# Kernel optimization log

Hardware: AMD Instinct MI355X
Metric: run time of the kernel (lower is better)

Reference implementation:

```python
import jax, jax.numpy as jnp
import numpy as np

CH, H, N, N_SSM, SEQ_L = 1, 1024, 64, 1024, 2048


def setup_inputs() -> dict:
    key = jax.random.key(0)
    ks = jax.random.split(key, 5)
    return {
        "C_ri": jax.random.normal(ks[0], (CH, H, N, 2), dtype=jnp.float32),
        "log_dt": jax.random.normal(ks[1], (H,), dtype=jnp.float32),
        "B_ri": jax.random.normal(ks[2], (N_SSM, N, 2), dtype=jnp.float32),
        "inv_A_real": jax.random.normal(ks[3], (N_SSM, N), dtype=jnp.float32),
        "A_imag": jax.random.normal(ks[4], (N_SSM, N), dtype=jnp.float32),
        "L": SEQ_L,
    }


def _kernel(C_ri, log_dt, B_ri, inv_A_real, A_imag, L):
    # Reconstruct complex params from real views (torch view_as_complex)
    C = C_ri[..., 0] + 1j * C_ri[..., 1]        # (CH, H, N) complex64
    B = B_ri[..., 0] + 1j * B_ri[..., 1]        # (n_ssm, N)
    A = -jnp.exp(inv_A_real) + 1j * A_imag      # (n_ssm, N), Re(A) < 0

    rep = log_dt.shape[0] // inv_A_real.shape[0]  # H // n_ssm
    B = jnp.tile(B, (rep, 1))                   # 't n -> (v t) n' : (H, N)
    A = jnp.tile(A, (rep, 1))                   # (H, N)

    dt = jnp.exp(log_dt)                        # (H,), rate = 1.0
    dtA = A * dt[:, None]                       # (H, N)

    # C <- B * C * dt / (1 - dtA/2)   (bilinear discretization of input/output)
    Ct = (B[None] * C) / (1.0 - dtA / 2) * dt[:, None]   # (CH, H, N)
    dA = (1.0 + dtA / 2) / (1.0 - dtA / 2)      # (H, N), |dA| < 1
    dA_log = jnp.log(dA)                        # (H, N)

    # log-Vandermonde: K[c,h,l] = 2 * Re( sum_n Ct[c,h,n] * exp(dA_log[h,n] * l) )
    l = jnp.arange(L, dtype=jnp.float32)
    V = jnp.exp(dA_log[:, :, None] * l)         # (H, N, L) complex
    K = 2.0 * jnp.einsum('chn,hnl->chl', Ct, V).real  # (CH, H, L)
    return K


def reference(C_ri, log_dt, B_ri, inv_A_real, A_imag, L):
    # state=None path: returns (K, K_state=None); we return K
    return _kernel(C_ri, log_dt, B_ri, inv_A_real, A_imag, L)
```

## Files before the change

### kernel.cpp

```cpp
#include <hip/hip_runtime.h>
#include <math.h>

#define CH 1
#define H 1024
#define NN 64
#define N_SSM 1024
#define SEQ_L 2048
#define TPB 256
#define LPT 8

typedef float v2f __attribute__((ext_vector_type(2)));

__global__ __launch_bounds__(TPB) void sskd_kernel(
    const float* __restrict__ C_ri, const float* __restrict__ log_dt,
    const float* __restrict__ B_ri, const float* __restrict__ inv_A_real,
    const float* __restrict__ A_imag, float* __restrict__ out)
{
    const int h   = blockIdx.x;
    const int tid = threadIdx.x;

    __shared__ __align__(8) float sCtr[NN], sCti[NN], sCdr[NN], sCdi[NN],
                                  sP[NN], sQ[NN], sLogr[NN], sThrev[NN];

    if (tid < NN) {
        const int n = tid;
        const float dt  = __expf(log_dt[h]);
        const float Ar  = -__expf(inv_A_real[h * NN + n]);
        const float Ai  = A_imag[h * NN + n];
        const float dtAr = Ar * dt, dtAi = Ai * dt;
        const float den_r = 1.0f - 0.5f * dtAr;
        const float den_i = -0.5f * dtAi;
        const float num_r = 1.0f + 0.5f * dtAr;
        const float num_i = 0.5f * dtAi;
        const float inv_den = 1.0f / (den_r * den_r + den_i * den_i);
        const float dA_r = (num_r * den_r + num_i * den_i) * inv_den;
        const float dA_i = (num_i * den_r - num_r * den_i) * inv_den;
        const int   bh = h % N_SSM;
        const float Br = B_ri[(bh * NN + n) * 2 + 0];
        const float Bi = B_ri[(bh * NN + n) * 2 + 1];
        const float Cr = C_ri[(h * NN + n) * 2 + 0];
        const float Ci = C_ri[(h * NN + n) * 2 + 1];
        const float BCr = Br * Cr - Bi * Ci;
        const float BCi = Br * Ci + Bi * Cr;
        const float sc = 2.0f * dt * inv_den;
        const float ctr = (BCr * den_r + BCi * den_i) * sc;
        const float cti = (BCi * den_r - BCr * den_i) * sc;
        sCtr[n] = ctr;
        sCti[n] = cti;
        sCdr[n] = ctr * dA_r - cti * dA_i;
        sCdi[n] = ctr * dA_i + cti * dA_r;
        const float q = dA_r * dA_r + dA_i * dA_i;
        sP[n] = 2.0f * dA_r;
        sQ[n] = q;
        sLogr[n]  = fmaxf(0.5f * __logf(q), -1.0e30f);
        sThrev[n] = atan2f(dA_i, dA_r) * 0.15915494309189535f;
    }
    __syncthreads();

    const float l0 = (float)(tid * LPT);
    v2f acc[LPT];
    #pragma unroll
    for (int k = 0; k < LPT; ++k) acc[k] = (v2f)(0.0f);

    #pragma unroll 2
    for (int m = 0; m < NN / 2; ++m) {
        const v2f logr  = *(const v2f*)&sLogr[2 * m];
        const v2f threv = *(const v2f*)&sThrev[2 * m];
        v2f e;
        e.x = __expf(logr.x * l0);
        e.y = __expf(logr.y * l0);
        v2f ph = threv * l0;
        ph.x -= floorf(ph.x);
        ph.y -= floorf(ph.y);
        float snx, csx, sny, csy;
        __sincosf(ph.x * 6.283185307179586f, &snx, &csx);
        __sincosf(ph.y * 6.283185307179586f, &sny, &csy);
        v2f wr, wi;
        wr.x = e.x * csx; wr.y = e.y * csy;
        wi.x = e.x * snx; wi.y = e.y * sny;

        const v2f ctr = *(const v2f*)&sCtr[2 * m];
        const v2f cti = *(const v2f*)&sCti[2 * m];
        const v2f cdr = *(const v2f*)&sCdr[2 * m];
        const v2f cdi = *(const v2f*)&sCdi[2 * m];
        const v2f p   = *(const v2f*)&sP[2 * m];
        const v2f q   = *(const v2f*)&sQ[2 * m];

        v2f x2 = ctr * wr - cti * wi;
        v2f x1 = cdr * wr - cdi * wi;
        acc[0] += x2;
        acc[1] += x1;
        #pragma unroll
        for (int k = 2; k < LPT; ++k) {
            const v2f xn = p * x1 - q * x2;
            acc[k] += xn;
            x2 = x1;
            x1 = xn;
        }
    }

    float4 o0, o1;
    o0.x = acc[0].x + acc[0].y;
    o0.y = acc[1].x + acc[1].y;
    o0.z = acc[2].x + acc[2].y;
    o0.w = acc[3].x + acc[3].y;
    o1.x = acc[4].x + acc[4].y;
    o1.y = acc[5].x + acc[5].y;
    o1.z = acc[6].x + acc[6].y;
    o1.w = acc[7].x + acc[7].y;
    float4* o = (float4*)(out + (size_t)h * SEQ_L + tid * LPT);
    o[0] = o0;
    o[1] = o1;
}

extern "C" void kernel_launch(void* const* d_in, const int* in_sizes, int n_in,
                              void* d_out, int out_size, void* d_ws, size_t ws_size,
                              hipStream_t stream) {
    const float* C_ri       = (const float*)d_in[0];
    const float* log_dt     = (const float*)d_in[1];
    const float* B_ri       = (const float*)d_in[2];
    const float* inv_A_real = (const float*)d_in[3];
    const float* A_imag     = (const float*)d_in[4];
    float* out = (float*)d_out;

    sskd_kernel<<<dim3(H), dim3(TPB), 0, stream>>>(
        C_ri, log_dt, B_ri, inv_A_real, A_imag, out);
}
```

Measured before the change: 78.20 us.

## Replace per-thread exp/sincos with precomputed power tables via repeated squaring

Each thread's starting power dA^(8*tid) is now built as the product of a coarse power (dA^(128*t1)) and a fine power (dA^(8*t0)), both precomputed into shared-memory tables by repeated complex squaring. This drops the per-term expf, floorf and sincos transcendentals from the inner loop and replaces them with extra shared-memory loads. The cost is a second table-building phase, an extra barrier and more LDS traffic. Forming high powers by repeated squaring can also lose accuracy compared with the log/exp form.

```diff
diff --git a/kernel.cpp b/kernel.cpp
--- a/kernel.cpp
+++ b/kernel.cpp
@@ -8,6 +8,7 @@
 #define SEQ_L 2048
 #define TPB 256
 #define LPT 8
+#define TSTR 68
 
 typedef float v2f __attribute__((ext_vector_type(2)));
 
@@ -19,8 +20,12 @@
     const int h   = blockIdx.x;
     const int tid = threadIdx.x;
 
-    __shared__ __align__(8) float sCtr[NN], sCti[NN], sCdr[NN], sCdi[NN],
-                                  sP[NN], sQ[NN], sLogr[NN], sThrev[NN];
+    __shared__ __align__(16) float sU1r[16][TSTR], sU1i[16][TSTR];
+    __shared__ __align__(16) float sVdr[16][TSTR], sVdi[16][TSTR];
+    __shared__ __align__(16) float sT0r[16][TSTR], sT0i[16][TSTR];
+    __shared__ __align__(16) float sP[NN], sQ[NN];
+    __shared__ __align__(16) float sW8r[NN], sW8i[NN], sW128r[NN], sW128i[NN];
+    __shared__ __align__(16) float sCtr[NN], sCti[NN], sCdr[NN], sCdi[NN];
 
     if (tid < NN) {
         const int n = tid;
@@ -45,49 +50,85 @@
         const float sc = 2.0f * dt * inv_den;
         const float ctr = (BCr * den_r + BCi * den_i) * sc;
         const float cti = (BCi * den_r - BCr * den_i) * sc;
-        sCtr[n] = ctr;
-        sCti[n] = cti;
+        sCtr[n] = ctr; sCti[n] = cti;
         sCdr[n] = ctr * dA_r - cti * dA_i;
         sCdi[n] = ctr * dA_i + cti * dA_r;
-        const float q = dA_r * dA_r + dA_i * dA_i;
         sP[n] = 2.0f * dA_r;
-        sQ[n] = q;
-        sLogr[n]  = fmaxf(0.5f * __logf(q), -1.0e30f);
-        sThrev[n] = atan2f(dA_i, dA_r) * 0.15915494309189535f;
+        sQ[n] = dA_r * dA_r + dA_i * dA_i;
+        float wr = dA_r * dA_r - dA_i * dA_i, wi = 2.0f * dA_r * dA_i;
+        float tr = wr * wr - wi * wi,         ti = 2.0f * wr * wi;
+        wr = tr * tr - ti * ti;               wi = 2.0f * tr * ti;
+        sW8r[n] = wr; sW8i[n] = wi;
+        tr = wr * wr - wi * wi;               ti = 2.0f * wr * wi;
+        wr = tr * tr - ti * ti;               wi = 2.0f * tr * ti;
+        tr = wr * wr - wi * wi;               ti = 2.0f * wr * wi;
+        wr = tr * tr - ti * ti;               wi = 2.0f * tr * ti;
+        sW128r[n] = wr; sW128i[n] = wi;
     }
     __syncthreads();
 
-    const float l0 = (float)(tid * LPT);
+    {
+        const int n = tid & 63;
+        const int g = tid >> 6;
+        {
+            const float wr = sW128r[n], wi = sW128i[n];
+            const float ctr = sCtr[n], cti = sCti[n];
+            const float cdr = sCdr[n], cdi = sCdi[n];
+            const float b2r = wr*wr - wi*wi,   b2i = 2.0f*wr*wi;
+            const float b4r = b2r*b2r - b2i*b2i, b4i = 2.0f*b2r*b2i;
+            const float b8r = b4r*b4r - b4i*b4i, b8i = 2.0f*b4r*b4i;
+            float Wr = 1.0f, Wi = 0.0f;
+            if (g & 1) { Wr = b4r; Wi = b4i; }
+            if (g & 2) { const float t = Wr*b8r - Wi*b8i; Wi = Wr*b8i + Wi*b8r; Wr = t; }
+            #pragma unroll
+            for (int i = 0; i < 4; ++i) {
+                const int t1 = 4 * g + i;
+                sU1r[t1][n] = ctr*Wr - cti*Wi;
+                sU1i[t1][n] = ctr*Wi + cti*Wr;
+                sVdr[t1][n] = cdr*Wr - cdi*Wi;
+                sVdi[t1][n] = cdr*Wi + cdi*Wr;
+                const float t = Wr*wr - Wi*wi; Wi = Wr*wi + Wi*wr; Wr = t;
+            }
+        }
+        {
+            const float ur = sW8r[n], ui = sW8i[n];
+            const float a2r = ur*ur - ui*ui,     a2i = 2.0f*ur*ui;
+            const float a4r = a2r*a2r - a2i*a2i, a4i = 2.0f*a2r*a2i;
+            const float a8r = a4r*a4r - a4i*a4i, a8i = 2.0f*a4r*a4i;
+            float Vr = 1.0f, Vi = 0.0f;
+            if (g & 1) { Vr = a4r; Vi = a4i; }
+            if (g & 2) { const float t = Vr*a8r - Vi*a8i; Vi = Vr*a8i + Vi*a8r; Vr = t; }
+            #pragma unroll
+            for (int i = 0; i < 4; ++i) {
+                const int t0 = 4 * g + i;
+                sT0r[t0][n] = Vr;
+                sT0i[t0][n] = Vi;
+                const float t = Vr*ur - Vi*ui; Vi = Vr*ui + Vi*ur; Vr = t;
+            }
+        }
+    }
+    __syncthreads();
+
+    const int t1 = tid >> 4;
+    const int t0 = tid & 15;
+
     v2f acc[LPT];
     #pragma unroll
     for (int k = 0; k < LPT; ++k) acc[k] = (v2f)(0.0f);
 
     #pragma unroll 2
     for (int m = 0; m < NN / 2; ++m) {
-        const v2f logr  = *(const v2f*)&sLogr[2 * m];
-        const v2f threv = *(const v2f*)&sThrev[2 * m];
-        v2f e;
-        e.x = __expf(logr.x * l0);
-        e.y = __expf(logr.y * l0);
-        v2f ph = threv * l0;
-        ph.x -= floorf(ph.x);
-        ph.y -= floorf(ph.y);
-        float snx, csx, sny, csy;
-        __sincosf(ph.x * 6.283185307179586f, &snx, &csx);
-        __sincosf(ph.y * 6.283185307179586f, &sny, &csy);
-        v2f wr, wi;
-        wr.x = e.x * csx; wr.y = e.y * csy;
-        wi.x = e.x * snx; wi.y = e.y * sny;
+        const v2f ur = *(const v2f*)&sU1r[t1][2 * m];
+        const v2f ui = *(const v2f*)&sU1i[t1][2 * m];
+        const v2f vr = *(const v2f*)&sVdr[t1][2 * m];
+        const v2f vi = *(const v2f*)&sVdi[t1][2 * m];
+        const v2f br = *(const v2f*)&sT0r[t0][2 * m];
+        const v2f bi = *(const v2f*)&sT0i[t0][2 * m];
+        const v2f p  = *(const v2f*)&sP[2 * m];
+        const v2f q  = *(const v2f*)&sQ[2 * m];
 
-        const v2f ctr = *(const v2f*)&sCtr[2 * m];
-        const v2f cti = *(const v2f*)&sCti[2 * m];
-        const v2f cdr = *(const v2f*)&sCdr[2 * m];
-        const v2f cdi = *(const v2f*)&sCdi[2 * m];
-        const v2f p   = *(const v2f*)&sP[2 * m];
-        const v2f q   = *(const v2f*)&sQ[2 * m];
-
-        v2f x2 = ctr * wr - cti * wi;
-        v2f x1 = cdr * wr - cdi * wi;
+        v2f x2 = ur * br - ui * bi;
+        v2f x1 = vr * br - vi * bi;
         acc[0] += x2;
         acc[1] += x1;
         #pragma unroll
```

Result: faster. 73.56 us (-5.9%).

## Replace per-thread exp/sincos with double-precision power tables and factored complex products

Applied to the files above, without the earlier changes.

Each thread no longer evaluates exp and sincos of dA^l. The kernel now precomputes powers of dA by repeated squaring in double precision and stores them in shared-memory tables. Each starting power is split into a coarse factor (W^256 times C, and a shifted ×W^8 copy) and a fine factor (W^16), so a complex multiply rebuilds the seed and the second-order recurrence runs two interleaved 8-step chains. Threads drop to 128 per block with 16 outputs each. This removes transcendental work and adds ILP, but costs double-precision setup, a second barrier, more LDS traffic and lower occupancy.

```diff
diff --git a/kernel.cpp b/kernel.cpp
--- a/kernel.cpp
+++ b/kernel.cpp
@@ -6,10 +6,13 @@
 #define NN 64
 #define N_SSM 1024
 #define SEQ_L 2048
-#define TPB 256
-#define LPT 8
+#define TPB 128
+#define LPT 16
 
 typedef float v2f __attribute__((ext_vector_type(2)));
+
+__device__ __forceinline__ v2f lo2(const float4 f) { v2f r; r.x = f.x; r.y = f.y; return r; }
+__device__ __forceinline__ v2f hi2(const float4 f) { v2f r; r.x = f.z; r.y = f.w; return r; }
 
 __global__ __launch_bounds__(TPB) void sskd_kernel(
     const float* __restrict__ C_ri, const float* __restrict__ log_dt,
@@ -19,98 +22,155 @@
     const int h   = blockIdx.x;
     const int tid = threadIdx.x;
 
-    __shared__ __align__(8) float sCtr[NN], sCti[NN], sCdr[NN], sCdi[NN],
-                                  sP[NN], sQ[NN], sLogr[NN], sThrev[NN];
+    __shared__ __align__(16) float4 sU1[8][33], sV1[8][33], sU8[8][33], sV8[8][33];
+    __shared__ __align__(16) float4 sT[16][33];
+    __shared__ __align__(16) float4 sPQ[32];
+    __shared__ double sW8r[NN], sW8i[NN], sW16r[NN], sW16i[NN], sW256r[NN], sW256i[NN];
+    __shared__ double sCtr[NN], sCti[NN], sCdr[NN], sCdi[NN];
 
     if (tid < NN) {
         const int n = tid;
-        const float dt  = __expf(log_dt[h]);
-        const float Ar  = -__expf(inv_A_real[h * NN + n]);
-        const float Ai  = A_imag[h * NN + n];
-        const float dtAr = Ar * dt, dtAi = Ai * dt;
-        const float den_r = 1.0f - 0.5f * dtAr;
-        const float den_i = -0.5f * dtAi;
-        const float num_r = 1.0f + 0.5f * dtAr;
-        const float num_i = 0.5f * dtAi;
-        const float inv_den = 1.0f / (den_r * den_r + den_i * den_i);
-        const float dA_r = (num_r * den_r + num_i * den_i) * inv_den;
-        const float dA_i = (num_i * den_r - num_r * den_i) * inv_den;
-        const int   bh = h % N_SSM;
-        const float Br = B_ri[(bh * NN + n) * 2 + 0];
-        const float Bi = B_ri[(bh * NN + n) * 2 + 1];
-        const float Cr = C_ri[(h * NN + n) * 2 + 0];
-        const float Ci = C_ri[(h * NN + n) * 2 + 1];
-        const float BCr = Br * Cr - Bi * Ci;
-        const float BCi = Br * Ci + Bi * Cr;
-        const float sc = 2.0f * dt * inv_den;
-        const float ctr = (BCr * den_r + BCi * den_i) * sc;
-        const float cti = (BCi * den_r - BCr * den_i) * sc;
-        sCtr[n] = ctr;
-        sCti[n] = cti;
-        sCdr[n] = ctr * dA_r - cti * dA_i;
-        sCdi[n] = ctr * dA_i + cti * dA_r;
-        const float q = dA_r * dA_r + dA_i * dA_i;
-        sP[n] = 2.0f * dA_r;
-        sQ[n] = q;
-        sLogr[n]  = fmaxf(0.5f * __logf(q), -1.0e30f);
-        sThrev[n] = atan2f(dA_i, dA_r) * 0.15915494309189535f;
+        const double dt = exp((double)log_dt[h]);
+        const double Ar = -exp((double)inv_A_real[h * NN + n]);
+        const double Ai = (double)A_imag[h * NN + n];
+        const double hr = 0.5 * Ar * dt, hi = 0.5 * Ai * dt;
+        const double den_r = 1.0 - hr, den_i = -hi;
+        const double num_r = 1.0 + hr, num_i = hi;
+        const double inv_den = 1.0 / (den_r * den_r + den_i * den_i);
+        const double dAr = (num_r * den_r + num_i * den_i) * inv_den;
+        const double dAi = (num_i * den_r - num_r * den_i) * inv_den;
+        const int    bh = h % N_SSM;
+        const double Br = B_ri[(bh * NN + n) * 2 + 0];
+        const double Bi = B_ri[(bh * NN + n) * 2 + 1];
+        const double Cr = C_ri[(h * NN + n) * 2 + 0];
+        const double Ci = C_ri[(h * NN + n) * 2 + 1];
+        const double BCr = Br * Cr - Bi * Ci;
+        const double BCi = Br * Ci + Bi * Cr;
+        const double sc = 2.0 * dt * inv_den;
+        const double ctr = (BCr * den_r + BCi * den_i) * sc;
+        const double cti = (BCi * den_r - BCr * den_i) * sc;
+        sCtr[n] = ctr; sCti[n] = cti;
+        sCdr[n] = ctr * dAr - cti * dAi;
+        sCdi[n] = ctr * dAi + cti * dAr;
+        float* pqp = (float*)&sPQ[n >> 1];
+        pqp[(n & 1)]     = (float)(2.0 * dAr);
+        pqp[2 + (n & 1)] = (float)(dAr * dAr + dAi * dAi);
+        double wr = dAr, wi = dAi, tr;
+        tr = wr * wr - wi * wi; wi = 2.0 * wr * wi; wr = tr;
+        tr = wr * wr - wi * wi; wi = 2.0 * wr * wi; wr = tr;
+        tr = wr * wr - wi * wi; wi = 2.0 * wr * wi; wr = tr;
+        sW8r[n] = wr; sW8i[n] = wi;
+        tr = wr * wr - wi * wi; wi = 2.0 * wr * wi; wr = tr;
+        sW16r[n] = wr; sW16i[n] = wi;
+        tr = wr * wr - wi * wi; wi = 2.0 * wr * wi; wr = tr;
+        tr = wr * wr - wi * wi; wi = 2.0 * wr * wi; wr = tr;
+        tr = wr * wr - wi * wi; wi = 2.0 * wr * wi; wr = tr;
+        tr = wr * wr - wi * wi; wi = 2.0 * wr * wi; wr = tr;
+        sW256r[n] = wr; sW256i[n] = wi;
     }
     __syncthreads();
 
-    const float l0 = (float)(tid * LPT);
+    {
+        const int n = tid & 63;
+        const int g = tid >> 6;
+        const int np = n >> 1, nc = n & 1;
+        {
+            const double ur = sW16r[n], ui = sW16i[n];
+            double Vr = 1.0, Vi = 0.0;
+            if (g) {
+                double ar = ur, ai = ui, t;
+                t = ar * ar - ai * ai; ai = 2.0 * ar * ai; ar = t;
+                t = ar * ar - ai * ai; ai = 2.0 * ar * ai; ar = t;
+                t = ar * ar - ai * ai; ai = 2.0 * ar * ai; ar = t;
+                Vr = ar; Vi = ai;
+            }
+            #pragma unroll
+            for (int i = 0; i < 8; ++i) {
+                float* bp = (float*)&sT[8 * g + i][np];
+                bp[nc] = (float)Vr; bp[2 + nc] = (float)Vi;
+                const double t = Vr * ur - Vi * ui; Vi = Vr * ui + Vi * ur; Vr = t;
+            }
+        }
+        {
+            const double wr = sW256r[n], wi = sW256i[n];
+            const double er = sW8r[n],  ei = sW8i[n];
+            const double ctr = sCtr[n], cti = sCti[n];
+            const double cdr = sCdr[n], cdi = sCdi[n];
+            double Wr = 1.0, Wi = 0.0;
+            if (g) {
+                double ar = wr, ai = wi, t;
+                t = ar * ar - ai * ai; ai = 2.0 * ar * ai; ar = t;
+                t = ar * ar - ai * ai; ai = 2.0 * ar * ai; ar = t;
+                Wr = ar; Wi = ai;
+            }
+            #pragma unroll
+            for (int i = 0; i < 4; ++i) {
+                const int t1 = 4 * g + i;
+                const double u1r = ctr * Wr - cti * Wi, u1i = ctr * Wi + cti * Wr;
+                const double v1r = cdr * Wr - cdi * Wi, v1i = cdr * Wi + cdi * Wr;
+                const double u8r = u1r * er - u1i * ei, u8i = u1r * ei + u1i * er;
+                const double v8r = v1r * er - v1i * ei, v8i = v1r * ei + v1i * er;
+                float* a = (float*)&sU1[t1][np]; a[nc] = (float)u1r; a[2 + nc] = (float)u1i;
+                float* b = (float*)&sV1[t1][np]; b[nc] = (float)v1r; b[2 + nc] = (float)v1i;
+                float* c = (float*)&sU8[t1][np]; c[nc] = (float)u8r; c[2 + nc] = (float)u8i;
+                float* d = (float*)&sV8[t1][np]; d[nc] = (float)v8r; d[2 + nc] = (float)v8i;
+                const double t = Wr * wr - Wi * wi; Wi = Wr * wi + Wi * wr; Wr = t;
+            }
+        }
+    }
+    __syncthreads();
+
+    const int t1 = tid >> 4;
+    const int t0 = tid & 15;
+
     v2f acc[LPT];
     #pragma unroll
     for (int k = 0; k < LPT; ++k) acc[k] = (v2f)(0.0f);
 
+    float4 u1 = sU1[t1][0], v1 = sV1[t1][0], u8 = sU8[t1][0], v8 = sV8[t1][0];
+    float4 tt = sT[t0][0],  pq = sPQ[0];
+
     #pragma unroll 2
     for (int m = 0; m < NN / 2; ++m) {
-        const v2f logr  = *(const v2f*)&sLogr[2 * m];
-        const v2f threv = *(const v2f*)&sThrev[2 * m];
-        v2f e;
-        e.x = __expf(logr.x * l0);
-        e.y = __expf(logr.y * l0);
-        v2f ph = threv * l0;
-        ph.x -= floorf(ph.x);
-        ph.y -= floorf(ph.y);
-        float snx, csx, sny, csy;
-        __sincosf(ph.x * 6.283185307179586f, &snx, &csx);
-        __sincosf(ph.y * 6.283185307179586f, &sny, &csy);
-        v2f wr, wi;
-        wr.x = e.x * csx; wr.y = e.y * csy;
-        wi.x = e.x * snx; wi.y = e.y * sny;
+        const int mn = (m + 1) & 31;
+        const float4 u1n = sU1[t1][mn], v1n = sV1[t1][mn];
+        const float4 u8n = sU8[t1][mn], v8n = sV8[t1][mn];
+        const float4 ttn = sT[t0][mn],  pqn = sPQ[mn];
 
-        const v2f ctr = *(const v2f*)&sCtr[2 * m];
-        const v2f cti = *(const v2f*)&sCti[2 * m];
-        const v2f cdr = *(const v2f*)&sCdr[2 * m];
-        const v2f cdi = *(const v2f*)&sCdi[2 * m];
-        const v2f p   = *(const v2f*)&sP[2 * m];
-        const v2f q   = *(const v2f*)&sQ[2 * m];
+        const v2f br = lo2(tt), bi = hi2(tt);
+        const v2f p  = lo2(pq), q  = hi2(pq);
 
-        v2f x2 = ctr * wr - cti * wi;
-        v2f x1 = cdr * wr - cdi * wi;
-        acc[0] += x2;
-        acc[1] += x1;
+        v2f xA2 = lo2(u1) * br - hi2(u1) * bi;
+        v2f xA1 = lo2(v1) * br - hi2(v1) * bi;
+        v2f xB2 = lo2(u8) * br - hi2(u8) * bi;
+        v2f xB1 = lo2(v8) * br - hi2(v8) * bi;
+        acc[0] += xA2; acc[1] += xA1;
+        acc[8] += xB2; acc[9] += xB1;
         #pragma unroll
-        for (int k = 2; k < LPT; ++k) {
-            const v2f xn = p * x1 - q * x2;
-            acc[k] += xn;
-            x2 = x1;
-            x1 = xn;
+        for (int k = 2; k < 8; ++k) {
+            const v2f xn = p * xA1 - q * xA2;
+            acc[k] += xn;     xA2 = xA1; xA1 = xn;
+            const v2f yn = p * xB1 - q * xB2;
+            acc[8 + k] += yn; xB2 = xB1; xB1 = yn;
         }
+
+        u1 = u1n; v1 = v1n; u8 = u8n; v8 = v8n; tt = ttn; pq = pqn;
     }
 
-    float4 o0, o1;
-    o0.x = acc[0].x + acc[0].y;
-    o0.y = acc[1].x + acc[1].y;
-    o0.z = acc[2].x + acc[2].y;
-    o0.w = acc[3].x + acc[3].y;
-    o1.x = acc[4].x + acc[4].y;
-    o1.y = acc[5].x + acc[5].y;
-    o1.z = acc[6].x + acc[6].y;
-    o1.w = acc[7].x + acc[7].y;
-    float4* o = (float4*)(out + (size_t)h * SEQ_L + tid * LPT);
-    o[0] = o0;
-    o[1] = o1;
+    float4 o;
+    float4* op = (float4*)(out + (size_t)h * SEQ_L + tid * LPT);
+    o.x = acc[0].x  + acc[0].y;  o.y = acc[1].x  + acc[1].y;
+    o.z = acc[2].x  + acc[2].y;  o.w = acc[3].x  + acc[3].y;
+    op[0] = o;
+    o.x = acc[4].x  + acc[4].y;  o.y = acc[5].x  + acc[5].y;
+    o.z = acc[6].x  + acc[6].y;  o.w = acc[7].x  + acc[7].y;
+    op[1] = o;
+    o.x = acc[8].x  + acc[8].y;  o.y = acc[9].x  + acc[9].y;
+    o.z = acc[10].x + acc[10].y; o.w = acc[11].x + acc[11].y;
+    op[2] = o;
+    o.x = acc[12].x + acc[12].y; o.y = acc[13].x + acc[13].y;
+    o.z = acc[14].x + acc[14].y; o.w = acc[15].x + acc[15].y;
+    op[3] = o;
 }
 
 extern "C" void kernel_launch(void* const* d_in, const int* in_sizes, int n_in,
```

Measured after the change: 75.18 us. -3.9%, faster.
